# Kernel tuning notes

Hardware: AMD Instinct MI355X
Metric: run time of the kernel (lower is better)

The kernel has to match this reference:

```python
import jax, jax.numpy as jnp
import numpy as np

B, T, D, NQ, NK, H = 2, 2048, 2048, 16, 4, 128
ROPE_THETA = 10000.0

def _timescale(head_dim, max_ts=ROPE_THETA, min_ts=1.0):
    frac = 2.0 * jnp.arange(head_dim // 2, dtype=jnp.float32) / head_dim
    return (min_ts * (max_ts / min_ts) ** frac).astype(jnp.float32)

def _apply_rope(x, pos):
    # x: [B,S,N,H], pos: [B,S] int
    ts = _timescale(x.shape[-1])
    sinu = pos.astype(jnp.float32)[..., None, None] / ts  # [B,S,1,H/2]
    sin, cos = jnp.sin(sinu), jnp.cos(sinu)
    x = x.astype(jnp.float32)
    x1, x2 = jnp.split(x, 2, axis=-1)
    return jnp.concatenate((x1 * cos - x2 * sin, x2 * cos + x1 * sin), axis=-1)

def setup_inputs() -> dict:
    key = jax.random.key(0)
    ks = jax.random.split(key, 5)
    X = jax.random.normal(ks[0], (B, T, D), dtype=jnp.float32)
    q_positions = jnp.broadcast_to(jnp.arange(T, dtype=jnp.int32), (B, T))
    s = 1.0 / np.sqrt(D)
    Wq = jax.random.normal(ks[1], (D, NQ, H), dtype=jnp.float32) * s
    Wk = jax.random.normal(ks[2], (D, NK, H), dtype=jnp.float32) * s
    Wv = jax.random.normal(ks[3], (D, NK, H), dtype=jnp.float32) * s
    Wo = jax.random.normal(ks[4], (NQ, H, D), dtype=jnp.float32) * (1.0 / np.sqrt(NQ * H))
    return {"X": X, "q_positions": q_positions, "Wq": Wq, "Wk": Wk, "Wv": Wv, "Wo": Wo}

def reference(X, q_positions, Wq, Wk, Wv, Wo):
    # Q/K/V projections
    q = jnp.einsum('btd,dnh->btnh', X, Wq)   # [B,T,NQ,H]
    k = jnp.einsum('bsd,dkh->bskh', X, Wk)   # [B,S,NK,H]
    v = jnp.einsum('bsd,dkh->bskh', X, Wv)
    # RoPE (kv_positions defaults to q_positions)
    q = _apply_rope(q, q_positions)
    k = _apply_rope(k, q_positions)
    # GQA causal SDPA, scale=1.0 (as in source)
    G = NQ // NK
    qg = q.reshape(B, T, NK, G, H)
    logits = jnp.einsum('btkgh,bskh->bkgts', qg, k)  # [B,NK,G,T,S]
    t_idx = jnp.arange(T)[:, None]
    s_idx = jnp.arange(T)[None, :]
    causal = (s_idx <= t_idx)
    logits = jnp.where(causal, logits, jnp.finfo(logits.dtype).min)
    probs = jax.nn.softmax(logits, axis=-1)
    attn = jnp.einsum('bkgts,bskh->btkgh', probs, v).reshape(B, T, NQ, H)
    out = jnp.einsum('btnh,nhd->btd', attn, Wo)
    return out.astype(X.dtype)
```

## Files before the change

### kernel.cpp

```cpp
#include <hip/hip_runtime.h>


typedef _Float16 half8 __attribute__((ext_vector_type(8)));
typedef float f32x4 __attribute__((ext_vector_type(4)));

#define GLOAD16(gp, lp) \
  __builtin_amdgcn_global_load_lds((__attribute__((address_space(1))) void*)(gp), \
                                   (__attribute__((address_space(3))) void*)(lp), 16, 0, 0)

#define WAIT_VM8() asm volatile("s_waitcnt vmcnt(8)" ::: "memory")
#define WAIT_VM0() asm volatile("s_waitcnt vmcnt(0)" ::: "memory")
#define BAR() asm volatile("s_barrier" ::: "memory")

static constexpr int T_   = 2048;
static constexpr int D_   = 2048;
static constexpr int NQ_  = 16;
static constexpr int NK_  = 4;
static constexpr int H_   = 128;
static constexpr int NQKV = 3072;
static constexpr int KOFF = 2048;
static constexpr int VOFF = 2560;


__global__ void cast_x_kernel(const float* __restrict__ in, _Float16* __restrict__ out) {
  int i = (blockIdx.x * 256 + threadIdx.x) * 4;
  float4 v = *reinterpret_cast<const float4*>(in + i);
  union { _Float16 h[4]; uint2 u; } p;
  p.h[0] = (_Float16)v.x; p.h[1] = (_Float16)v.y;
  p.h[2] = (_Float16)v.z; p.h[3] = (_Float16)v.w;
  *reinterpret_cast<uint2*>(out + i) = p.u;
}

__global__ void transpose_cast_kernel(const float* __restrict__ in,
                                      _Float16* __restrict__ out, int ncols) {
  __shared__ float tile[32][33];
  int n0 = blockIdx.x * 32, k0 = blockIdx.y * 32;
  int tx = threadIdx.x, ty = threadIdx.y;
#pragma unroll
  for (int i = 0; i < 32; i += 8)
    tile[ty + i][tx] = in[(size_t)(k0 + ty + i) * ncols + (n0 + tx)];
  __syncthreads();
#pragma unroll
  for (int i = 0; i < 32; i += 8)
    out[(size_t)(n0 + ty + i) * 2048 + (k0 + tx)] = (_Float16)tile[tx][ty + i];
}

__global__ void rope_kernel(_Float16* __restrict__ qkv, const int* __restrict__ pos) {
  int idx = blockIdx.x * 256 + threadIdx.x;
  int h = idx & 63;
  int head = (idx >> 6) % 20;
  int m = idx / (64 * 20);
  float p = (float)pos[m];
  float freq = expf(-0.14391156831f * (float)h);
  float a = p * freq;
  float s, c;
  sincosf(a, &s, &c);
  int col = (head < 16) ? (head * H_ + h) : (KOFF + (head - 16) * H_ + h);
  _Float16* ptr = qkv + (size_t)m * NQKV + col;
  float x1 = (float)ptr[0], x2 = (float)ptr[64];
  ptr[0]  = (_Float16)(x1 * c - x2 * s);
  ptr[64] = (_Float16)(x2 * c + x1 * s);
}

__global__ void vtrans_kernel(const _Float16* __restrict__ qkv, _Float16* __restrict__ vt) {
  __shared__ _Float16 tile[32][33];
  int t0 = blockIdx.x * 32, h0 = blockIdx.y * 32;
  int slab = blockIdx.z;
  int tx = threadIdx.x, ty = threadIdx.y;
  int b = slab >> 2, kh = slab & 3;
#pragma unroll
  for (int i = 0; i < 32; i += 8)
    tile[ty + i][tx] = qkv[(size_t)(b * T_ + t0 + ty + i) * NQKV + VOFF + kh * H_ + h0 + tx];
  __syncthreads();
#pragma unroll
  for (int i = 0; i < 32; i += 8)
    vt[(size_t)(slab * H_ + h0 + ty + i) * T_ + (t0 + tx)] = tile[tx][ty + i];
}


template <int OUT_F32>
__global__ __launch_bounds__(256, 2) void gemm_kernel(const _Float16* __restrict__ A,
                                                      const _Float16* __restrict__ Bt,
                                                      void* __restrict__ Cout, int N, int K) {
  __shared__ __align__(16) _Float16 As[128 * 64];
  __shared__ __align__(16) _Float16 Bs[128 * 64];
  const int tid = threadIdx.x;
  const int wave = tid >> 6, lane = tid & 63;
  const int lg = lane >> 4, lm = lane & 15;
  const int brow = blockIdx.y * 128, bcol = blockIdx.x * 128;
  const int wr = wave >> 1, wc = wave & 1;
  f32x4 acc[4][4] = {};
  for (int k0 = 0; k0 < K; k0 += 64) {
#pragma unroll
    for (int j = 0; j < 4; ++j) {
      int U = j * 256 + tid;
      int row = U >> 3, u = U & 7;
      int us = u ^ (row & 7);
      GLOAD16(A + (size_t)(brow + row) * K + k0 + us * 8, (char*)As + ((j * 256 + wave * 64) << 4));
      GLOAD16(Bt + (size_t)(bcol + row) * K + k0 + us * 8, (char*)Bs + ((j * 256 + wave * 64) << 4));
    }
    __syncthreads();
#pragma unroll
    for (int kk = 0; kk < 2; ++kk) {
      half8 af[4], bf[4];
#pragma unroll
      for (int m = 0; m < 4; ++m) {
        int row = wr * 64 + m * 16 + lm;
        int u = (kk * 4 + lg) ^ (row & 7);
        af[m] = *reinterpret_cast<const half8*>(As + row * 64 + u * 8);
      }
#pragma unroll
      for (int n = 0; n < 4; ++n) {
        int row = wc * 64 + n * 16 + lm;
        int u = (kk * 4 + lg) ^ (row & 7);
        bf[n] = *reinterpret_cast<const half8*>(Bs + row * 64 + u * 8);
      }
#pragma unroll
      for (int m = 0; m < 4; ++m)
#pragma unroll
        for (int n = 0; n < 4; ++n)
          acc[m][n] = __builtin_amdgcn_mfma_f32_16x16x32_f16(af[m], bf[n], acc[m][n], 0, 0, 0);
    }
    __syncthreads();
  }
#pragma unroll
  for (int m = 0; m < 4; ++m)
#pragma unroll
    for (int n = 0; n < 4; ++n)
#pragma unroll
      for (int r = 0; r < 4; ++r) {
        size_t row = brow + wr * 64 + m * 16 + lg * 4 + r;
        size_t col = bcol + wc * 64 + n * 16 + lm;
        if constexpr (OUT_F32) ((float*)Cout)[row * N + col] = acc[m][n][r];
        else ((_Float16*)Cout)[row * N + col] = (_Float16)acc[m][n][r];
      }
}


__global__ __launch_bounds__(256, 2) void attn_kernel(const _Float16* __restrict__ qkv,
                                                      const _Float16* __restrict__ vt,
                                                      _Float16* __restrict__ attn) {
  __shared__ __align__(16) _Float16 Ks[2][64 * 128];
  __shared__ __align__(16) _Float16 Vs[2][128 * 64];
  __shared__ __align__(16) _Float16 Ps[4][16 * 64];
  const int bid = blockIdx.x;
  const int swz = (bid & 7) * 64 + (bid >> 3);
  const int chunk = swz >> 6;
  const int b = chunk >> 2, kh = chunk & 3;
  const int n = kh * 4 + ((swz >> 4) & 3);
  const int p = swz & 15;
  const int tid = threadIdx.x, wave = tid >> 6, lane = tid & 63;
  const int lg = lane >> 4, lm = lane & 15;

  auto stage = [&](int j, int buf) {
    const int s0 = j * 64;
    char* Kb = (char*)&Ks[buf][0];
    char* Vb = (char*)&Vs[buf][0];
#pragma unroll
    for (int jj = 0; jj < 4; ++jj) {
      int U = jj * 256 + tid;
      int srow = U >> 4, u = U & 15;
      int us = u ^ (srow & 15);
      GLOAD16(qkv + (size_t)(b * T_ + s0 + srow) * NQKV + KOFF + kh * H_ + us * 8,
              Kb + ((jj * 256 + wave * 64) << 4));
    }
#pragma unroll
    for (int jj = 0; jj < 4; ++jj) {
      int U = jj * 256 + tid;
      int hrow = U >> 3, u = U & 7;
      int us = u ^ (hrow & 7);
      GLOAD16(vt + (size_t)((b * NK_ + kh) * H_ + hrow) * T_ + s0 + us * 8,
              Vb + ((jj * 256 + wave * 64) << 4));
    }
  };

  for (int ph = 0; ph < 2; ++ph) {
    const int t = ph ? (31 - p) : p;
    const int qbase = t * 64 + wave * 16;

    half8 qf[4];
    const _Float16* qptr = qkv + (size_t)(b * T_ + qbase + lm) * NQKV + n * H_;
#pragma unroll
    for (int kk = 0; kk < 4; ++kk)
      qf[kk] = *reinterpret_cast<const half8*>(qptr + kk * 32 + lg * 8);

    f32x4 o[8] = {};
    float mrow[4], lrow[4];
#pragma unroll
    for (int r = 0; r < 4; ++r) { mrow[r] = -1e30f; lrow[r] = 0.f; }

    const int nkv = t + 1;
    stage(0, 0);
    for (int it = 0; it < nkv; ++it) {
      const int cur = it & 1;
      if (it + 1 < nkv) { stage(it + 1, cur ^ 1); WAIT_VM8(); }
      else              { WAIT_VM0(); }
      BAR();
      const _Float16* Kt = &Ks[cur][0];
      const _Float16* Vt2 = &Vs[cur][0];

      f32x4 S[4];
      __builtin_amdgcn_s_setprio(1);
#pragma unroll
      for (int ns = 0; ns < 4; ++ns) {
        half8 kf[4];
        int srow = ns * 16 + lm;
#pragma unroll
        for (int kk = 0; kk < 4; ++kk) {
          int u = (kk * 4 + lg) ^ (srow & 15);
          kf[kk] = *reinterpret_cast<const half8*>(Kt + srow * 128 + u * 8);
        }
        f32x4 a = {0.f, 0.f, 0.f, 0.f};
#pragma unroll
        for (int kk = 0; kk < 4; ++kk)
          a = __builtin_amdgcn_mfma_f32_16x16x32_f16(qf[kk], kf[kk], a, 0, 0, 0);
        S[ns] = a;
      }
      __builtin_amdgcn_s_setprio(0);

      if (it == t) {
#pragma unroll
        for (int ns = 0; ns < 4; ++ns)
#pragma unroll
          for (int r = 0; r < 4; ++r) {
            int q = qbase + lg * 4 + r;
            int s = t * 64 + ns * 16 + lm;
            if (s > q) S[ns][r] = -1e30f;
          }
      }

#pragma unroll
      for (int r = 0; r < 4; ++r) {
        float pm = fmaxf(fmaxf(S[0][r], S[1][r]), fmaxf(S[2][r], S[3][r]));
        pm = fmaxf(pm, __shfl_xor(pm, 1));
        pm = fmaxf(pm, __shfl_xor(pm, 2));
        pm = fmaxf(pm, __shfl_xor(pm, 4));
        pm = fmaxf(pm, __shfl_xor(pm, 8));
        float mo = mrow[r];
        float mn = fmaxf(mo, pm);
        float sc = __expf(mo - mn);
        mrow[r] = mn;
        float ps = 0.f;
#pragma unroll
        for (int ns = 0; ns < 4; ++ns) {
          float pv = __expf(S[ns][r] - mn);
          S[ns][r] = pv;
          ps += pv;
        }
        ps += __shfl_xor(ps, 1);
        ps += __shfl_xor(ps, 2);
        ps += __shfl_xor(ps, 4);
        ps += __shfl_xor(ps, 8);
        lrow[r] = lrow[r] * sc + ps;
#pragma unroll
        for (int nh = 0; nh < 8; ++nh) o[nh][r] *= sc;
        int q = lg * 4 + r;
#pragma unroll
        for (int ns = 0; ns < 4; ++ns) {
          int s = ns * 16 + lm;
          Ps[wave][q * 64 + (((s >> 3) ^ (q & 7)) << 3) + (s & 7)] = (_Float16)S[ns][r];
        }
      }

      __builtin_amdgcn_s_setprio(1);
#pragma unroll
      for (int kk2 = 0; kk2 < 2; ++kk2) {
        int qrow = lm;
        int up = (kk2 * 4 + lg) ^ (qrow & 7);
        half8 pa = *reinterpret_cast<const half8*>(&Ps[wave][qrow * 64 + up * 8]);
#pragma unroll
        for (int nh = 0; nh < 8; ++nh) {
          int hrow = nh * 16 + lm;
          int u = (kk2 * 4 + lg) ^ (hrow & 7);
          half8 vf = *reinterpret_cast<const half8*>(Vt2 + hrow * 64 + u * 8);
          o[nh] = __builtin_amdgcn_mfma_f32_16x16x32_f16(pa, vf, o[nh], 0, 0, 0);
        }
      }
      __builtin_amdgcn_s_setprio(0);
      BAR();
    }

#pragma unroll
    for (int r = 0; r < 4; ++r) {
      float inv = 1.f / lrow[r];
      int q = qbase + lg * 4 + r;
      _Float16* optr = attn + ((size_t)(b * T_ + q) * NQ_ + n) * H_ + lm;
#pragma unroll
      for (int nh = 0; nh < 8; ++nh)
        optr[nh * 16] = (_Float16)(o[nh][r] * inv);
    }
  }
}


extern "C" void kernel_launch(void* const* d_in, const int* in_sizes, int n_in,
                              void* d_out, int out_size, void* d_ws, size_t ws_size,
                              hipStream_t stream) {
  const float* X  = (const float*)d_in[0];
  const int* pos  = (const int*)d_in[1];
  const float* Wq = (const float*)d_in[2];
  const float* Wk = (const float*)d_in[3];
  const float* Wv = (const float*)d_in[4];
  const float* Wo = (const float*)d_in[5];

  _Float16* Xh    = (_Float16*)d_ws;
  _Float16* Wqkvt = Xh + (size_t)4096 * 2048;
  _Float16* Wot   = Wqkvt + (size_t)3072 * 2048;
  _Float16* QKV   = Wot + (size_t)2048 * 2048;
  _Float16* Vt    = QKV + (size_t)4096 * 3072;
  _Float16* Attn  = Vt + (size_t)8 * 128 * 2048;

  dim3 tb(32, 8);
  cast_x_kernel<<<8192, 256, 0, stream>>>(X, Xh);
  transpose_cast_kernel<<<dim3(64, 64), tb, 0, stream>>>(Wq, Wqkvt, 2048);
  transpose_cast_kernel<<<dim3(16, 64), tb, 0, stream>>>(Wk, Wqkvt + (size_t)2048 * 2048, 512);
  transpose_cast_kernel<<<dim3(16, 64), tb, 0, stream>>>(Wv, Wqkvt + (size_t)2560 * 2048, 512);
  transpose_cast_kernel<<<dim3(64, 64), tb, 0, stream>>>(Wo, Wot, 2048);

  gemm_kernel<0><<<dim3(24, 32), 256, 0, stream>>>(Xh, Wqkvt, QKV, NQKV, 2048);
  rope_kernel<<<20480, 256, 0, stream>>>(QKV, pos);
  vtrans_kernel<<<dim3(64, 4, 8), tb, 0, stream>>>(QKV, Vt);
  attn_kernel<<<512, 256, 0, stream>>>(QKV, Vt, Attn);
  gemm_kernel<1><<<dim3(16, 32), 256, 0, stream>>>(Attn, Wot, d_out, 2048, 2048);
}
```

Before: 233.6 us.

## Transpose QK^T MFMA, use exp2 softmax with lazy rescaling

Swaps the QK MFMA operands so each lane holds one query row's scores, which cuts the softmax row reductions from four shuffle chains per row to two cross-group shuffles. Q is pre-scaled by log2(e) so exp2 can replace expf. The running max is only rescaled when some row's new max exceeds the old one by more than a threshold, which skips most rescales of the O accumulator. P is stored to LDS as packed half4 writes. The cost is extra shuffles to broadcast the scale factors and a small precision risk from the fp16 rescaling of Q and from the lazy max.

```diff
diff --git a/kernel.cpp b/kernel.cpp
--- a/kernel.cpp
+++ b/kernel.cpp
@@ -2,6 +2,7 @@
 
 
 typedef _Float16 half8 __attribute__((ext_vector_type(8)));
+typedef _Float16 half4 __attribute__((ext_vector_type(4)));
 typedef float f32x4 __attribute__((ext_vector_type(4)));
 
 #define GLOAD16(gp, lp) \
@@ -181,13 +182,15 @@
     half8 qf[4];
     const _Float16* qptr = qkv + (size_t)(b * T_ + qbase + lm) * NQKV + n * H_;
 #pragma unroll
-    for (int kk = 0; kk < 4; ++kk)
-      qf[kk] = *reinterpret_cast<const half8*>(qptr + kk * 32 + lg * 8);
+    for (int kk = 0; kk < 4; ++kk) {
+      half8 qr = *reinterpret_cast<const half8*>(qptr + kk * 32 + lg * 8);
+#pragma unroll
+      for (int j = 0; j < 8; ++j)
+        qf[kk][j] = (_Float16)((float)qr[j] * 1.4426950408889634f);
+    }
 
     f32x4 o[8] = {};
-    float mrow[4], lrow[4];
-#pragma unroll
-    for (int r = 0; r < 4; ++r) { mrow[r] = -1e30f; lrow[r] = 0.f; }
+    float mrow_s = -1e30f, lrow_s = 0.f;
 
     const int nkv = t + 1;
     stage(0, 0);
@@ -213,61 +216,72 @@
         f32x4 a = {0.f, 0.f, 0.f, 0.f};
 #pragma unroll
         for (int kk = 0; kk < 4; ++kk)
-          a = __builtin_amdgcn_mfma_f32_16x16x32_f16(qf[kk], kf[kk], a, 0, 0, 0);
+          a = __builtin_amdgcn_mfma_f32_16x16x32_f16(kf[kk], qf[kk], a, 0, 0, 0);
         S[ns] = a;
       }
       __builtin_amdgcn_s_setprio(0);
 
       if (it == t) {
+        const int q = qbase + lm;
 #pragma unroll
         for (int ns = 0; ns < 4; ++ns)
 #pragma unroll
           for (int r = 0; r < 4; ++r) {
-            int q = qbase + lg * 4 + r;
-            int s = t * 64 + ns * 16 + lm;
+            int s = t * 64 + ns * 16 + lg * 4 + r;
             if (s > q) S[ns][r] = -1e30f;
           }
       }
 
-#pragma unroll
-      for (int r = 0; r < 4; ++r) {
-        float pm = fmaxf(fmaxf(S[0][r], S[1][r]), fmaxf(S[2][r], S[3][r]));
-        pm = fmaxf(pm, __shfl_xor(pm, 1));
-        pm = fmaxf(pm, __shfl_xor(pm, 2));
-        pm = fmaxf(pm, __shfl_xor(pm, 4));
-        pm = fmaxf(pm, __shfl_xor(pm, 8));
-        float mo = mrow[r];
-        float mn = fmaxf(mo, pm);
-        float sc = __expf(mo - mn);
-        mrow[r] = mn;
-        float ps = 0.f;
-#pragma unroll
-        for (int ns = 0; ns < 4; ++ns) {
-          float pv = __expf(S[ns][r] - mn);
+      float pm0 = fmaxf(fmaxf(S[0][0], S[0][1]), fmaxf(S[0][2], S[0][3]));
+      float pm1 = fmaxf(fmaxf(S[1][0], S[1][1]), fmaxf(S[1][2], S[1][3]));
+      float pm2 = fmaxf(fmaxf(S[2][0], S[2][1]), fmaxf(S[2][2], S[2][3]));
+      float pm3 = fmaxf(fmaxf(S[3][0], S[3][1]), fmaxf(S[3][2], S[3][3]));
+      float pm = fmaxf(fmaxf(pm0, pm1), fmaxf(pm2, pm3));
+      pm = fmaxf(pm, __shfl_xor(pm, 16));
+      pm = fmaxf(pm, __shfl_xor(pm, 32));
+
+      if (__any(pm > mrow_s + 14.f)) {
+        float mn = fmaxf(mrow_s, pm);
+        float sc = __builtin_amdgcn_exp2f(mrow_s - mn);
+        mrow_s = mn;
+        lrow_s *= sc;
+        float scr[4];
+#pragma unroll
+        for (int r = 0; r < 4; ++r) scr[r] = __shfl(sc, lg * 4 + r);
+#pragma unroll
+        for (int nh = 0; nh < 8; ++nh)
+#pragma unroll
+          for (int r = 0; r < 4; ++r) o[nh][r] *= scr[r];
+      }
+
+      const float m = mrow_s;
+      float ps = 0.f;
+#pragma unroll
+      for (int ns = 0; ns < 4; ++ns)
+#pragma unroll
+        for (int r = 0; r < 4; ++r) {
+          float pv = __builtin_amdgcn_exp2f(S[ns][r] - m);
           S[ns][r] = pv;
           ps += pv;
         }
-        ps += __shfl_xor(ps, 1);
-        ps += __shfl_xor(ps, 2);
-        ps += __shfl_xor(ps, 4);
-        ps += __shfl_xor(ps, 8);
-        lrow[r] = lrow[r] * sc + ps;
-#pragma unroll
-        for (int nh = 0; nh < 8; ++nh) o[nh][r] *= sc;
-        int q = lg * 4 + r;
-#pragma unroll
-        for (int ns = 0; ns < 4; ++ns) {
-          int s = ns * 16 + lm;
-          Ps[wave][q * 64 + (((s >> 3) ^ (q & 7)) << 3) + (s & 7)] = (_Float16)S[ns][r];
-        }
+      ps += __shfl_xor(ps, 16);
+      ps += __shfl_xor(ps, 32);
+      lrow_s += ps;
+
+#pragma unroll
+      for (int ns = 0; ns < 4; ++ns) {
+        half4 pk;
+#pragma unroll
+        for (int r = 0; r < 4; ++r) pk[r] = (_Float16)S[ns][r];
+        int u = (2 * ns + (lg >> 1)) ^ (lm & 7);
+        *reinterpret_cast<half4*>(&Ps[wave][lm * 64 + u * 8 + (lg & 1) * 4]) = pk;
       }
 
       __builtin_amdgcn_s_setprio(1);
 #pragma unroll
       for (int kk2 = 0; kk2 < 2; ++kk2) {
-        int qrow = lm;
-        int up = (kk2 * 4 + lg) ^ (qrow & 7);
-        half8 pa = *reinterpret_cast<const half8*>(&Ps[wave][qrow * 64 + up * 8]);
+        int up = (kk2 * 4 + lg) ^ (lm & 7);
+        half8 pa = *reinterpret_cast<const half8*>(&Ps[wave][lm * 64 + up * 8]);
 #pragma unroll
         for (int nh = 0; nh < 8; ++nh) {
           int hrow = nh * 16 + lm;
@@ -280,14 +294,16 @@
       BAR();
     }
 
+    float linv[4];
+#pragma unroll
+    for (int r = 0; r < 4; ++r) linv[r] = 1.f / __shfl(lrow_s, lg * 4 + r);
 #pragma unroll
     for (int r = 0; r < 4; ++r) {
-      float inv = 1.f / lrow[r];
       int q = qbase + lg * 4 + r;
       _Float16* optr = attn + ((size_t)(b * T_ + q) * NQ_ + n) * H_ + lm;
 #pragma unroll
       for (int nh = 0; nh < 8; ++nh)
-        optr[nh * 16] = (_Float16)(o[nh][r] * inv);
+        optr[nh * 16] = (_Float16)(o[nh][r] * linv[r]);
     }
   }
 }
```

After: 209.0 us. 10.5% less time.
